# Kernel optimization log

Hardware: AMD Instinct MI355X
Metric: run time of the kernel (lower is better)

Reference implementation:

```python
import jax, jax.numpy as jnp
import numpy as np

S = 28        # number of atoms / per-atom MLPs (2 N + 14 C + 12 H)
NAT = 28      # atoms the descriptor derivatives span
FEA_IN = 2048
HIDDEN = 1024


def setup_inputs() -> dict:
    key = jax.random.key(0)
    k0, k1, k2, k3 = jax.random.split(key, 4)
    des = jax.random.normal(k0, (S, FEA_IN), dtype=jnp.float32)
    der = jax.random.normal(k1, (S, NAT, 3, FEA_IN), dtype=jnp.float32) * 0.1
    # kaiming_normal for ReLU: std = sqrt(2 / fan_in); biases filled with 0
    W1 = jax.random.normal(k2, (S, HIDDEN, FEA_IN), dtype=jnp.float32) * np.sqrt(2.0 / FEA_IN)
    b1 = jnp.zeros((S, HIDDEN), dtype=jnp.float32)
    W2 = jax.random.normal(k3, (S, 1, HIDDEN), dtype=jnp.float32) * np.sqrt(2.0 / HIDDEN)
    b2 = jnp.zeros((S, 1), dtype=jnp.float32)
    return {"des": des, "der": der, "W1": W1, "b1": b1, "W2": W2, "b2": b2}


def _energy(des, W1, b1, W2, b2):
    # 28 independent 2-layer MLPs, batched over the species axis s.
    h = jax.nn.relu(jnp.einsum('sf,shf->sh', des, W1) + b1)   # [S, H]
    e = jnp.einsum('sh,sh->s', h, W2[:, 0, :]) + b2[:, 0]      # [S]
    return jnp.sum(e)                                          # scalar total energy


def reference(des, der, W1, b1, W2, b2):
    # calc_ene_pred: sum of the 28 per-atom MLP energies.
    # calc_force_pred: de/dD per species, then F = -einsum('jkl,l->jk') summed over species.
    ene_scalar, de_dD = jax.value_and_grad(
        lambda d: _energy(d, W1, b1, W2, b2))(des)             # de_dD: [S, FEA_IN]
    force = -jnp.einsum('sjkl,sl->jk', der, de_dD)             # [NAT, 3]
    ene_pred = ene_scalar.reshape(1)                           # matches summed [1]-shaped outputs
    return ene_pred, force
```

## Files before the change

### kernel.cpp

```cpp
#include <hip/hip_runtime.h>

#define S_ATOMS 28
#define FEA 2048
#define HID 1024
#define JK 84
#define HB_PER_S 64
#define ENE_SLOTS 256
#define NBLK2 (S_ATOMS * JK / 4)

typedef float floatx4 __attribute__((ext_vector_type(4)));

__global__ __launch_bounds__(256) void bpnn_k1(
    const float* __restrict__ des, const float* __restrict__ W1,
    const float* __restrict__ b1,  const float* __restrict__ W2,
    float* __restrict__ g, float* __restrict__ ene_slots)
{
    const int s    = blockIdx.x / HB_PER_S;
    const int hb   = blockIdx.x % HB_PER_S;
    const int wave = threadIdx.x >> 6;
    const int lane = threadIdx.x & 63;

    const float* desS = des + (size_t)s * FEA;
    floatx4 d[8];
#pragma unroll
    for (int c = 0; c < 8; ++c)
        d[c] = *reinterpret_cast<const floatx4*>(desS + c * 256 + lane * 4);

    floatx4 gacc[8];
#pragma unroll
    for (int c = 0; c < 8; ++c) gacc[c] = (floatx4){0.f, 0.f, 0.f, 0.f};
    float eacc = 0.f;

    const int h0 = hb * 16 + wave * 4;
#pragma unroll
    for (int r = 0; r < 4; ++r) {
        const int h = h0 + r;
        const float* w = W1 + ((size_t)s * HID + h) * FEA;
        floatx4 wv[8];
#pragma unroll
        for (int c = 0; c < 8; ++c)
            wv[c] = __builtin_nontemporal_load(
                reinterpret_cast<const floatx4*>(w + c * 256 + lane * 4));
        float a0 = 0.f, a1 = 0.f, a2 = 0.f, a3 = 0.f;
#pragma unroll
        for (int c = 0; c < 8; ++c) {
            a0 = fmaf(wv[c].x, d[c].x, a0);
            a1 = fmaf(wv[c].y, d[c].y, a1);
            a2 = fmaf(wv[c].z, d[c].z, a2);
            a3 = fmaf(wv[c].w, d[c].w, a3);
        }
        float dot = (a0 + a1) + (a2 + a3);
#pragma unroll
        for (int m = 1; m < 64; m <<= 1)
            dot += __shfl_xor(dot, m, 64);
        const float hpre = dot + b1[s * HID + h];
        if (hpre > 0.f) {
            const float c2 = W2[s * HID + h];
            eacc = fmaf(hpre, c2, eacc);
#pragma unroll
            for (int c = 0; c < 8; ++c) {
                gacc[c].x = fmaf(c2, wv[c].x, gacc[c].x);
                gacc[c].y = fmaf(c2, wv[c].y, gacc[c].y);
                gacc[c].z = fmaf(c2, wv[c].z, gacc[c].z);
                gacc[c].w = fmaf(c2, wv[c].w, gacc[c].w);
            }
        }
    }

    __shared__ float gs[4][FEA];
    __shared__ float es[4];
    if (lane == 0) es[wave] = eacc;
#pragma unroll
    for (int c = 0; c < 8; ++c) {
        gs[wave][c * 256 +   0 + lane] = gacc[c].x;
        gs[wave][c * 256 +  64 + lane] = gacc[c].y;
        gs[wave][c * 256 + 128 + lane] = gacc[c].z;
        gs[wave][c * 256 + 192 + lane] = gacc[c].w;
    }
    __syncthreads();
    for (int p = threadIdx.x; p < FEA; p += 256) {
        const float v = (gs[0][p] + gs[1][p]) + (gs[2][p] + gs[3][p]);
        const int c = p >> 8;
        const int i = (p & 255) >> 6;
        const int l = p & 63;
        atomicAdd(&g[(size_t)s * FEA + c * 256 + l * 4 + i], v);
    }
    if (threadIdx.x == 0)
        atomicAdd(&ene_slots[blockIdx.x & (ENE_SLOTS - 1)], es[0] + es[1] + es[2] + es[3]);
}

__global__ __launch_bounds__(256) void bpnn_k2(
    const float* __restrict__ der, const float* __restrict__ g,
    const float* __restrict__ b2,  const float* __restrict__ ene_slots,
    float* __restrict__ out)
{
    if (blockIdx.x == NBLK2) {
        const int tid = threadIdx.x;
        if (tid < 64) {
            float e = ene_slots[tid] + ene_slots[tid + 64] +
                      ene_slots[tid + 128] + ene_slots[tid + 192];
#pragma unroll
            for (int m = 1; m < 64; m <<= 1)
                e += __shfl_xor(e, m, 64);
            if (tid == 0) {
                float bs = 0.f;
                for (int s = 0; s < S_ATOMS; ++s) bs += b2[s];
                out[0] = e + bs;
            }
        }
        return;
    }
    const int wave = threadIdx.x >> 6;
    const int lane = threadIdx.x & 63;
    const int id = blockIdx.x * 4 + wave;
    const int s  = id / JK;
    const int jk = id % JK;
    const float* dr = der + ((size_t)s * JK + jk) * FEA;
    const float* gr = g + (size_t)s * FEA;
    float a0 = 0.f, a1 = 0.f, a2 = 0.f, a3 = 0.f;
#pragma unroll
    for (int c = 0; c < 8; ++c) {
        const floatx4 a = __builtin_nontemporal_load(
            reinterpret_cast<const floatx4*>(dr + c * 256 + lane * 4));
        const floatx4 b = *reinterpret_cast<const floatx4*>(gr + c * 256 + lane * 4);
        a0 = fmaf(a.x, b.x, a0);
        a1 = fmaf(a.y, b.y, a1);
        a2 = fmaf(a.z, b.z, a2);
        a3 = fmaf(a.w, b.w, a3);
    }
    float acc = (a0 + a1) + (a2 + a3);
#pragma unroll
    for (int m = 1; m < 64; m <<= 1)
        acc += __shfl_xor(acc, m, 64);
    if (lane == 0)
        atomicAdd(&out[1 + jk], -acc);
}

extern "C" void kernel_launch(void* const* d_in, const int* in_sizes, int n_in,
                              void* d_out, int out_size, void* d_ws, size_t ws_size,
                              hipStream_t stream) {
    const float* des = (const float*)d_in[0];
    const float* der = (const float*)d_in[1];
    const float* W1  = (const float*)d_in[2];
    const float* b1  = (const float*)d_in[3];
    const float* W2  = (const float*)d_in[4];
    const float* b2  = (const float*)d_in[5];
    float* out = (float*)d_out;

    float* g         = (float*)d_ws;
    float* ene_slots = g + S_ATOMS * FEA;

    hipMemsetAsync(d_ws, 0, (size_t)(S_ATOMS * FEA + ENE_SLOTS) * sizeof(float), stream);
    hipMemsetAsync(d_out, 0, (size_t)out_size * sizeof(float), stream);

    bpnn_k1<<<S_ATOMS * HB_PER_S, 256, 0, stream>>>(des, W1, b1, W2, g, ene_slots);
    bpnn_k2<<<NBLK2 + 1, 256, 0, stream>>>(der, g, b2, ene_slots, out);
}
```

Baseline: 364.5 us.

## Replace global atomic gradient accumulation with per-block partials and a reduction kernel

```diff
diff --git a/kernel.cpp b/kernel.cpp
--- a/kernel.cpp
+++ b/kernel.cpp
@@ -5,15 +5,16 @@
 #define HID 1024
 #define JK 84
 #define HB_PER_S 64
-#define ENE_SLOTS 256
+#define NBLK1 (S_ATOMS * HB_PER_S)
 #define NBLK2 (S_ATOMS * JK / 4)
 
 typedef float floatx4 __attribute__((ext_vector_type(4)));
 
+
 __global__ __launch_bounds__(256) void bpnn_k1(
     const float* __restrict__ des, const float* __restrict__ W1,
     const float* __restrict__ b1,  const float* __restrict__ W2,
-    float* __restrict__ g, float* __restrict__ ene_slots)
+    float* __restrict__ g_part, float* __restrict__ ene_part)
 {
     const int s    = blockIdx.x / HB_PER_S;
     const int hb   = blockIdx.x % HB_PER_S;
@@ -78,27 +79,49 @@
         gs[wave][c * 256 + 192 + lane] = gacc[c].w;
     }
     __syncthreads();
-    for (int p = threadIdx.x; p < FEA; p += 256) {
+    float* part = g_part + (size_t)blockIdx.x * FEA;
+#pragma unroll
+    for (int q = 0; q < 8; ++q) {
+        const int p = q * 256 + threadIdx.x;
         const float v = (gs[0][p] + gs[1][p]) + (gs[2][p] + gs[3][p]);
-        const int c = p >> 8;
-        const int i = (p & 255) >> 6;
-        const int l = p & 63;
-        atomicAdd(&g[(size_t)s * FEA + c * 256 + l * 4 + i], v);
+        __builtin_nontemporal_store(v, &part[p]);
     }
     if (threadIdx.x == 0)
-        atomicAdd(&ene_slots[blockIdx.x & (ENE_SLOTS - 1)], es[0] + es[1] + es[2] + es[3]);
+        ene_part[blockIdx.x] = (es[0] + es[1]) + (es[2] + es[3]);
+}
+
+__global__ __launch_bounds__(256) void bpnn_k1r(
+    const float* __restrict__ g_part, float* __restrict__ g_p)
+{
+    const int s     = blockIdx.x >> 3;
+    const int chunk = blockIdx.x & 7;
+    const int p     = chunk * 256 + threadIdx.x;
+    const float* base = g_part + (size_t)s * HB_PER_S * FEA + p;
+    float a0 = 0.f, a1 = 0.f, a2 = 0.f, a3 = 0.f;
+#pragma unroll
+    for (int hb = 0; hb < HB_PER_S; hb += 4) {
+        a0 += __builtin_nontemporal_load(&base[(size_t)(hb    ) * FEA]);
+        a1 += __builtin_nontemporal_load(&base[(size_t)(hb + 1) * FEA]);
+        a2 += __builtin_nontemporal_load(&base[(size_t)(hb + 2) * FEA]);
+        a3 += __builtin_nontemporal_load(&base[(size_t)(hb + 3) * FEA]);
+    }
+    g_p[s * FEA + p] = (a0 + a1) + (a2 + a3);
 }
 
 __global__ __launch_bounds__(256) void bpnn_k2(
-    const float* __restrict__ der, const float* __restrict__ g,
-    const float* __restrict__ b2,  const float* __restrict__ ene_slots,
+    const float* __restrict__ der, const float* __restrict__ g_p,
+    const float* __restrict__ b2,  const float* __restrict__ ene_part,
     float* __restrict__ out)
 {
     if (blockIdx.x == NBLK2) {
         const int tid = threadIdx.x;
+        float e = 0.f;
+        for (int i = tid; i < NBLK1; i += 256) e += ene_part[i];
+        __shared__ float red[256];
+        red[tid] = e;
+        __syncthreads();
         if (tid < 64) {
-            float e = ene_slots[tid] + ene_slots[tid + 64] +
-                      ene_slots[tid + 128] + ene_slots[tid + 192];
+            e = (red[tid] + red[tid + 64]) + (red[tid + 128] + red[tid + 192]);
 #pragma unroll
             for (int m = 1; m < 64; m <<= 1)
                 e += __shfl_xor(e, m, 64);
@@ -116,17 +139,20 @@
     const int s  = id / JK;
     const int jk = id % JK;
     const float* dr = der + ((size_t)s * JK + jk) * FEA;
-    const float* gr = g + (size_t)s * FEA;
+    const float* gp = g_p + (size_t)s * FEA;
     float a0 = 0.f, a1 = 0.f, a2 = 0.f, a3 = 0.f;
 #pragma unroll
     for (int c = 0; c < 8; ++c) {
         const floatx4 a = __builtin_nontemporal_load(
             reinterpret_cast<const floatx4*>(dr + c * 256 + lane * 4));
-        const floatx4 b = *reinterpret_cast<const floatx4*>(gr + c * 256 + lane * 4);
-        a0 = fmaf(a.x, b.x, a0);
-        a1 = fmaf(a.y, b.y, a1);
-        a2 = fmaf(a.z, b.z, a2);
-        a3 = fmaf(a.w, b.w, a3);
+        const float bx = gp[c * 256 +       lane];
+        const float by = gp[c * 256 +  64 + lane];
+        const float bz = gp[c * 256 + 128 + lane];
+        const float bw = gp[c * 256 + 192 + lane];
+        a0 = fmaf(a.x, bx, a0);
+        a1 = fmaf(a.y, by, a1);
+        a2 = fmaf(a.z, bz, a2);
+        a3 = fmaf(a.w, bw, a3);
     }
     float acc = (a0 + a1) + (a2 + a3);
 #pragma unroll
@@ -147,12 +173,13 @@
     const float* b2  = (const float*)d_in[5];
     float* out = (float*)d_out;
 
-    float* g         = (float*)d_ws;
-    float* ene_slots = g + S_ATOMS * FEA;
+    float* g_p      = (float*)d_ws;
+    float* g_part   = g_p + S_ATOMS * FEA;
+    float* ene_part = g_part + (size_t)NBLK1 * FEA;
 
-    hipMemsetAsync(d_ws, 0, (size_t)(S_ATOMS * FEA + ENE_SLOTS) * sizeof(float), stream);
     hipMemsetAsync(d_out, 0, (size_t)out_size * sizeof(float), stream);
 
-    bpnn_k1<<<S_ATOMS * HB_PER_S, 256, 0, stream>>>(des, W1, b1, W2, g, ene_slots);
-    bpnn_k2<<<NBLK2 + 1, 256, 0, stream>>>(der, g, b2, ene_slots, out);
+    bpnn_k1 <<<NBLK1,      256, 0, stream>>>(des, W1, b1, W2, g_part, ene_part);
+    bpnn_k1r<<<S_ATOMS * 8, 256, 0, stream>>>(g_part, g_p);
+    bpnn_k2 <<<NBLK2 + 1,  256, 0, stream>>>(der, g_p, b2, ene_part, out);
 }
```

Result: faster. 337.8 us (-7.3%).
